# Performance work log

Hardware: AMD Instinct MI355X
Metric: run time of the kernel (lower is better)

## Reference

```python
import jax, jax.numpy as jnp
import numpy as np

EMBED_DIM = 1024
NUM_HEADS = 16
HEAD_DIM = EMBED_DIM // NUM_HEADS


def setup_inputs() -> dict:
    key = jax.random.key(0)
    ks = jax.random.split(key, 5)
    B, T = 2, 2048
    scale = 1.0 / np.sqrt(EMBED_DIM)
    x = jax.random.normal(ks[0], (B, T, EMBED_DIM), dtype=jnp.float32)
    W_qkv = jax.random.normal(ks[1], (EMBED_DIM, 3 * EMBED_DIM), dtype=jnp.float32) * scale
    b_qkv = jnp.zeros((3 * EMBED_DIM,), dtype=jnp.float32)
    W_out = jax.random.normal(ks[2], (EMBED_DIM, EMBED_DIM), dtype=jnp.float32) * scale
    b_out = jnp.zeros((EMBED_DIM,), dtype=jnp.float32)
    return {"x": x, "W_qkv": W_qkv, "b_qkv": b_qkv, "W_out": W_out, "b_out": b_out}


def reference(x, W_qkv, b_qkv, W_out, b_out):
    B, T, E = x.shape
    H, D = NUM_HEADS, HEAD_DIM
    qkv = x @ W_qkv + b_qkv  # [B,T,3E]
    q, k, v = jnp.split(qkv, 3, axis=-1)
    # [B,T,E] -> [B,H,T,D]
    q = q.reshape(B, T, H, D).transpose(0, 2, 1, 3)
    k = k.reshape(B, T, H, D).transpose(0, 2, 1, 3)
    v = v.reshape(B, T, H, D).transpose(0, 2, 1, 3)
    scores = jnp.einsum('bhqd,bhkd->bhqk', q, k) / jnp.sqrt(jnp.float32(D))
    causal = jnp.tril(jnp.ones((T, T), dtype=bool))  # True = keep
    scores = jnp.where(causal[None, None], scores, jnp.float32(-jnp.inf))
    attn = jax.nn.softmax(scores, axis=-1)  # dropout=0.0 (eval mode)
    out = jnp.einsum('bhqk,bhkd->bhqd', attn, v)
    out = out.transpose(0, 2, 1, 3).reshape(B, T, E)
    return out @ W_out + b_out
```

## Files before the change

kernel.cpp:

```cpp
#include <hip/hip_runtime.h>
#include <hip/hip_bf16.h>
#include <stdint.h>

typedef unsigned short u16;
typedef __attribute__((ext_vector_type(8))) short short8;
typedef __attribute__((ext_vector_type(4))) float f32x4;

#define T_SEQ 2048
#define EMB   1024
#define NH    16
#define HD    64

__device__ __forceinline__ u16 f2bf(float f) {
    union { float f; uint32_t u; } x; x.f = f;
    uint32_t u = x.u;
    uint32_t r = u + 0x7fffu + ((u >> 16) & 1u);
    return (u16)(r >> 16);
}

__device__ __forceinline__ uint32_t cvtpk(float a, float b) {
    uint32_t r;
    asm("v_cvt_pk_bf16_f32 %0, %1, %2" : "=v"(r) : "v"(a), "v"(b));
    return r;
}

__device__ __forceinline__ void gld16(const void* g, void* l) {
    __builtin_amdgcn_global_load_lds(
        (const __attribute__((address_space(1))) void*)g,
        (__attribute__((address_space(3))) void*)l, 16, 0, 0);
}

__global__ __launch_bounds__(256) void cast_bf16_kernel(const float* __restrict__ in,
                                                        u16* __restrict__ out, int n4) {
    int i = blockIdx.x * 256 + threadIdx.x;
    if (i < n4) {
        float4 v = ((const float4*)in)[i];
        ((uint2*)out)[i] = make_uint2(cvtpk(v.x, v.y), cvtpk(v.z, v.w));
    }
}

__global__ __launch_bounds__(256) void transpose_cast_kernel(const float* __restrict__ W,
                                                             u16* __restrict__ Wt,
                                                             int K, int N) {
    __shared__ float tile[32][33];
    int n0 = blockIdx.x * 32, k0 = blockIdx.y * 32;
    int tx = threadIdx.x, ty = threadIdx.y;
#pragma unroll
    for (int i = 0; i < 4; i++)
        tile[ty + i * 8][tx] = W[(k0 + ty + i * 8) * N + n0 + tx];
    __syncthreads();
#pragma unroll
    for (int i = 0; i < 4; i++)
        Wt[(size_t)(n0 + ty + i * 8) * K + k0 + tx] = f2bf(tile[tx][ty + i * 8]);
}

__device__ __forceinline__ void gemm_tile(const u16* __restrict__ A, const u16* __restrict__ Bt,
                                          int m0, int n0, f32x4 (&acc)[4][4],
                                          u16* As, u16* Bs, int tid) {
    const int lane = tid & 63;
    const int wid  = tid >> 6;
    const int wr = wid >> 1, wc = wid & 1;
    const int g = lane >> 4, r = lane & 15;
#pragma unroll
    for (int m = 0; m < 4; m++)
#pragma unroll
        for (int n = 0; n < 4; n++) acc[m][n] = (f32x4){0.f, 0.f, 0.f, 0.f};

    const int srow = tid >> 2;
    const int skb  = (tid & 3) * 8;
    const u16* ag = A  + (size_t)(m0 + srow) * 1024 + skb;
    const u16* bg = Bt + (size_t)(n0 + srow) * 1024 + skb;
    char* asl = (char*)As + tid * 16;
    char* bsl = (char*)Bs + tid * 16;

    auto stage = [&](int buf, int kk) {
        gld16(ag + kk,             asl + buf * 8192);
        gld16(ag + kk + 64 * 1024, asl + buf * 8192 + 4096);
        gld16(bg + kk,             bsl + buf * 8192);
        gld16(bg + kk + 64 * 1024, bsl + buf * 8192 + 4096);
    };

    stage(0, 0);
    for (int it = 0; it < 32; ++it) {
        const int cur = it & 1;
        __syncthreads();
        if (it < 31) stage(cur ^ 1, (it + 1) * 32);
        const u16* as = As + cur * 4096;
        const u16* bs = Bs + cur * 4096;
        short8 af[4], bf[4];
#pragma unroll
        for (int m = 0; m < 4; m++) af[m] = *(const short8*)&as[(wr * 64 + m * 16 + r) * 32 + g * 8];
#pragma unroll
        for (int n = 0; n < 4; n++) bf[n] = *(const short8*)&bs[(wc * 64 + n * 16 + r) * 32 + g * 8];
#pragma unroll
        for (int m = 0; m < 4; m++)
#pragma unroll
            for (int n = 0; n < 4; n++)
                acc[m][n] = __builtin_amdgcn_mfma_f32_16x16x32_bf16(af[m], bf[n], acc[m][n], 0, 0, 0);
    }
}

__global__ __launch_bounds__(256) void gemm_qkv_kernel(const u16* __restrict__ A, const u16* __restrict__ Bt,
                                                       const float* __restrict__ bias,
                                                       u16* __restrict__ Qo, u16* __restrict__ Ko,
                                                       u16* __restrict__ VTo) {
    __shared__ __align__(16) u16 As[2][128 * 32];
    __shared__ __align__(16) u16 Bs[2][128 * 32];
    int tid = threadIdx.x;
    int m0 = blockIdx.x * 128, n0 = blockIdx.y * 128;
    f32x4 acc[4][4];
    gemm_tile(A, Bt, m0, n0, acc, &As[0][0], &Bs[0][0], tid);

    int lane = tid & 63, wid = tid >> 6;
    int wr = wid >> 1, wc = wid & 1, g = lane >> 4, r = lane & 15;
#pragma unroll
    for (int m = 0; m < 4; m++) {
#pragma unroll
        for (int n = 0; n < 4; n++) {
            int col = n0 + wc * 64 + n * 16 + r;
            float bv = bias[col];
            int which = col >> 10;
            int e = col & 1023;
            int h = e >> 6, d = e & 63;
            int row0 = m0 + wr * 64 + m * 16 + g * 4;
            int b = row0 >> 11, t0 = row0 & 2047;
            if (which == 2) {
                uint2 pk;
                pk.x = cvtpk(acc[m][n][0] + bv, acc[m][n][1] + bv);
                pk.y = cvtpk(acc[m][n][2] + bv, acc[m][n][3] + bv);
                *(uint2*)&VTo[(((size_t)(b * NH + h)) * HD + d) * T_SEQ + t0] = pk;
            } else {
                u16* dst = which ? Ko : Qo;
                float sc = which ? 1.0f : 0.18033688011112042f;
#pragma unroll
                for (int j = 0; j < 4; j++)
                    dst[(((size_t)(b * NH + h)) * T_SEQ + t0 + j) * HD + d] = f2bf((acc[m][n][j] + bv) * sc);
            }
        }
    }
}

__global__ __launch_bounds__(256) void gemm_out_kernel(const u16* __restrict__ A, const u16* __restrict__ Bt,
                                                       const float* __restrict__ bias,
                                                       float* __restrict__ out) {
    __shared__ __align__(16) u16 As[2][128 * 32];
    __shared__ __align__(16) u16 Bs[2][128 * 32];
    int tid = threadIdx.x;
    int m0 = blockIdx.x * 128, n0 = blockIdx.y * 128;
    f32x4 acc[4][4];
    gemm_tile(A, Bt, m0, n0, acc, &As[0][0], &Bs[0][0], tid);

    int lane = tid & 63, wid = tid >> 6;
    int wr = wid >> 1, wc = wid & 1, g = lane >> 4, r = lane & 15;
#pragma unroll
    for (int m = 0; m < 4; m++) {
#pragma unroll
        for (int n = 0; n < 4; n++) {
            int col = n0 + wc * 64 + n * 16 + r;
            float bv = bias[col];
#pragma unroll
            for (int j = 0; j < 4; j++) {
                int row = m0 + wr * 64 + m * 16 + g * 4 + j;
                out[(size_t)row * 1024 + col] = acc[m][n][j] + bv;
            }
        }
    }
}

__global__ __launch_bounds__(512) void attn_kernel(const u16* __restrict__ Q, const u16* __restrict__ K,
                                                   const u16* __restrict__ VT, u16* __restrict__ O) {
    __shared__ __align__(16) char smem[43008];
    u16* Kl = (u16*)smem;
    u16* Vl = (u16*)(smem + 16384);
    u16 (*Ps)[16][40] = (u16(*)[16][40])(smem + 32768);

    const int tid = threadIdx.x;
    const int lane = tid & 63, wid = tid >> 6;
    const int g = lane >> 4, r = lane & 15;
    const int rg = wid & 3, kh = wid >> 2;
    const int bid = blockIdx.x;
    const int qt = 31 - (bid >> 5);
    const int bh = bid & 31;
    const int b = bh >> 4, h = bh & 15;
    const u16* Qb  = Q  + (size_t)bh * T_SEQ * HD;
    const u16* Kb  = K  + (size_t)bh * T_SEQ * HD;
    const u16* VTb = VT + (size_t)bh * HD * T_SEQ;
    u16 (*myPs)[40] = Ps[wid];
    const float NEGINF = -__builtin_inff();

    int koff[2][2], voff[4];
#pragma unroll
    for (int nt = 0; nt < 2; nt++)
#pragma unroll
        for (int hh = 0; hh < 2; hh++)
            koff[nt][hh] = ((kh * 2 + nt) * 16 + r) * 128 + ((((hh * 4 + g) ^ (r & 7)) << 4));
#pragma unroll
    for (int dt = 0; dt < 4; dt++)
        voff[dt] = (dt * 16 + r) * 128 + ((((kh * 4 + g) ^ (r & 7)) << 4));

    const int srow = tid >> 3;
    const int sm = (tid & 7) ^ (srow & 7);
    const u16* kgp = Kb + srow * HD + sm * 8;
    const u16* vgp = VTb + (size_t)srow * T_SEQ + sm * 8;
    char* kld = (char*)Kl + tid * 16;
    char* vld = (char*)Vl + tid * 16;
    auto stage = [&](int buf, int k0) {
        gld16(kgp + (size_t)k0 * HD, kld + (buf << 13));
        gld16(vgp + k0, vld + (buf << 13));
    };

    short8 onesf;
#pragma unroll
    for (int i = 0; i < 8; i++) onesf[i] = (short)0x3F80;

    const int q0 = qt * 64;
    const int q  = q0 + rg * 16 + r;

    stage(0, 0);

    short8 qf0 = *(const short8*)&Qb[(size_t)q * HD + 8 * g];
    short8 qf1 = *(const short8*)&Qb[(size_t)q * HD + 32 + 8 * g];

    float mrun = -1e30f, srun = 0.f;
    f32x4 o[4];
#pragma unroll
    for (int dt = 0; dt < 4; dt++) o[dt] = (f32x4){0.f, 0.f, 0.f, 0.f};

    for (int kv = 0; kv <= qt; kv++) {
        const int cur = kv & 1;
        const int k0 = kv * 64;
        __syncthreads();
        if (kv < qt) stage(cur ^ 1, k0 + 64);

        const char* kb = (const char*)Kl + (cur << 13);
        const char* vb = (const char*)Vl + (cur << 13);

        f32x4 s[2];
        __builtin_amdgcn_s_setprio(1);
#pragma unroll
        for (int nt = 0; nt < 2; nt++) {
            f32x4 z = (f32x4){0.f, 0.f, 0.f, 0.f};
            z = __builtin_amdgcn_mfma_f32_16x16x32_bf16(*(const short8*)(kb + koff[nt][0]), qf0, z, 0, 0, 0);
            z = __builtin_amdgcn_mfma_f32_16x16x32_bf16(*(const short8*)(kb + koff[nt][1]), qf1, z, 0, 0, 0);
            s[nt] = z;
        }
        __builtin_amdgcn_s_setprio(0);

        if (kv == qt) {
#pragma unroll
            for (int nt = 0; nt < 2; nt++) {
                int kbi = k0 + kh * 32 + nt * 16 + 4 * g;
#pragma unroll
                for (int j = 0; j < 4; j++)
                    if (kbi + j > q) s[nt][j] = NEGINF;
            }
        }

        float t0 = fmaxf(fmaxf(s[0][0], s[0][1]), s[0][2]);
        float t1 = fmaxf(fmaxf(s[0][3], s[1][0]), s[1][1]);
        float t2 = fmaxf(s[1][2], s[1][3]);
        float mt = fmaxf(fmaxf(t0, t1), t2);
        mt = fmaxf(mt, __shfl_xor(mt, 16));
        mt = fmaxf(mt, __shfl_xor(mt, 32));

        if (mt > mrun + 8.f) {
            float corr = __builtin_exp2f(mrun - mt);
            mrun = mt;
            srun *= corr;
#pragma unroll
            for (int dt = 0; dt < 4; dt++)
#pragma unroll
                for (int j = 0; j < 4; j++) o[dt][j] *= corr;
        }

#pragma unroll
        for (int nt = 0; nt < 2; nt++)
#pragma unroll
            for (int j = 0; j < 4; j++)
                s[nt][j] = __builtin_exp2f(s[nt][j] - mrun);

#pragma unroll
        for (int nt = 0; nt < 2; nt++) {
            uint2 pk;
            pk.x = cvtpk(s[nt][0], s[nt][1]);
            pk.y = cvtpk(s[nt][2], s[nt][3]);
            *(uint2*)&myPs[r][nt * 16 + 4 * g] = pk;
        }
        short8 pf = *(short8*)&myPs[r][8 * g];

        __builtin_amdgcn_s_setprio(1);
#pragma unroll
        for (int dt = 0; dt < 4; dt++)
            o[dt] = __builtin_amdgcn_mfma_f32_16x16x32_bf16(*(const short8*)(vb + voff[dt]), pf, o[dt], 0, 0, 0);
        f32x4 zs = (f32x4){0.f, 0.f, 0.f, 0.f};
        zs = __builtin_amdgcn_mfma_f32_16x16x32_bf16(onesf, pf, zs, 0, 0, 0);
        __builtin_amdgcn_s_setprio(0);
        srun += zs[0];
    }

    __syncthreads();
    float* mb = ((float*)smem) + ((rg * 64 + lane) * 18);
    if (kh) {
#pragma unroll
        for (int dt = 0; dt < 4; dt++) *(f32x4*)&mb[dt * 4] = o[dt];
        mb[16] = mrun;
        mb[17] = srun;
    }
    __syncthreads();
    if (!kh) {
        float m1 = mb[16], l1 = mb[17];
        float mm = fmaxf(mrun, m1);
        float c0 = __builtin_exp2f(mrun - mm);
        float c1 = __builtin_exp2f(m1 - mm);
        float inv = 1.f / (srun * c0 + l1 * c1);
        float s0 = c0 * inv, s1 = c1 * inv;
#pragma unroll
        for (int dt = 0; dt < 4; dt++) {
            f32x4 o1 = *(const f32x4*)&mb[dt * 4];
            uint2 pk;
            pk.x = cvtpk(o[dt][0] * s0 + o1[0] * s1, o[dt][1] * s0 + o1[1] * s1);
            pk.y = cvtpk(o[dt][2] * s0 + o1[2] * s1, o[dt][3] * s0 + o1[3] * s1);
            *(uint2*)&O[(((size_t)(b * T_SEQ + q)) * NH + h) * HD + dt * 16 + 4 * g] = pk;
        }
    }
}

extern "C" void kernel_launch(void* const* d_in, const int* in_sizes, int n_in,
                              void* d_out, int out_size, void* d_ws, size_t ws_size,
                              hipStream_t stream) {
    const float* x     = (const float*)d_in[0];
    const float* W_qkv = (const float*)d_in[1];
    const float* b_qkv = (const float*)d_in[2];
    const float* W_out = (const float*)d_in[3];
    const float* b_out = (const float*)d_in[4];
    float* out = (float*)d_out;

    char* ws = (char*)d_ws;
    u16* xb    = (u16*)(ws);
    u16* wqkvt = (u16*)(ws + 8388608);
    u16* woutt = (u16*)(ws + 14680064);
    u16* Qp    = (u16*)(ws + 16777216);
    u16* Kp    = (u16*)(ws + 25165824);
    u16* VTp   = (u16*)(ws + 33554432);
    u16* attnb = (u16*)(ws);

    cast_bf16_kernel<<<4096, 256, 0, stream>>>(x, xb, 1048576);
    transpose_cast_kernel<<<dim3(96, 32), dim3(32, 8), 0, stream>>>(W_qkv, wqkvt, 1024, 3072);
    transpose_cast_kernel<<<dim3(32, 32), dim3(32, 8), 0, stream>>>(W_out, woutt, 1024, 1024);
    gemm_qkv_kernel<<<dim3(32, 24), 256, 0, stream>>>(xb, wqkvt, b_qkv, Qp, Kp, VTp);
    attn_kernel<<<1024, 512, 0, stream>>>(Qp, Kp, VTp, attnb);
    gemm_out_kernel<<<dim3(32, 8), 256, 0, stream>>>(attnb, woutt, b_out, out);
}
```

Before: 126.3 us.

## Fuse prep kernels into one launch and shrink output GEMM tile to 64x128

Merges the x cast and both weight transpose-casts into a single prep kernel, saving two kernel launches. The output projection GEMM moves from 128x128 tiles over 256 blocks to 64x128 tiles over 512 blocks, with its own staging loop, so more CUs are busy on the 4096x1024 output. The attention kernel's shared memory becomes separate typed arrays, and the softmax merge buffer now aliases Kl. The smaller GEMM tile lowers per-block data reuse, and the prep kernel adds branching per block.

```diff
diff --git a/kernel.cpp b/kernel.cpp
--- a/kernel.cpp
+++ b/kernel.cpp
@@ -30,28 +30,31 @@
         (__attribute__((address_space(3))) void*)l, 16, 0, 0);
 }
 
-__global__ __launch_bounds__(256) void cast_bf16_kernel(const float* __restrict__ in,
-                                                        u16* __restrict__ out, int n4) {
-    int i = blockIdx.x * 256 + threadIdx.x;
-    if (i < n4) {
-        float4 v = ((const float4*)in)[i];
-        ((uint2*)out)[i] = make_uint2(cvtpk(v.x, v.y), cvtpk(v.z, v.w));
-    }
-}
-
-__global__ __launch_bounds__(256) void transpose_cast_kernel(const float* __restrict__ W,
-                                                             u16* __restrict__ Wt,
-                                                             int K, int N) {
+__global__ __launch_bounds__(256) void prep_kernel(const float* __restrict__ x, u16* __restrict__ xb,
+                                                   const float* __restrict__ Wq, u16* __restrict__ Wqt,
+                                                   const float* __restrict__ Wo, u16* __restrict__ Wot) {
     __shared__ float tile[32][33];
-    int n0 = blockIdx.x * 32, k0 = blockIdx.y * 32;
-    int tx = threadIdx.x, ty = threadIdx.y;
+    const int bid = blockIdx.x;
+    if (bid < 4096) {
+        int i = bid * 256 + threadIdx.x;
+        float4 v = ((const float4*)x)[i];
+        ((uint2*)xb)[i] = make_uint2(cvtpk(v.x, v.y), cvtpk(v.z, v.w));
+        return;
+    }
+    int t = bid - 4096;
+    const float* W; u16* Wt; int N;
+    if (t < 3072) { W = Wq; Wt = Wqt; N = 3072; }
+    else          { W = Wo; Wt = Wot; N = 1024; t -= 3072; }
+    const int ntiles = N >> 5;
+    const int n0 = (t % ntiles) * 32, k0 = (t / ntiles) * 32;
+    const int tx = threadIdx.x & 31, ty = threadIdx.x >> 5;
 #pragma unroll
     for (int i = 0; i < 4; i++)
-        tile[ty + i * 8][tx] = W[(k0 + ty + i * 8) * N + n0 + tx];
+        tile[ty + i * 8][tx] = W[(size_t)(k0 + ty + i * 8) * N + n0 + tx];
     __syncthreads();
 #pragma unroll
     for (int i = 0; i < 4; i++)
-        Wt[(size_t)(n0 + ty + i * 8) * K + k0 + tx] = f2bf(tile[tx][ty + i * 8]);
+        Wt[(size_t)(n0 + ty + i * 8) * 1024 + k0 + tx] = f2bf(tile[tx][ty + i * 8]);
 }
 
 __device__ __forceinline__ void gemm_tile(const u16* __restrict__ A, const u16* __restrict__ Bt,
@@ -143,24 +146,60 @@
 __global__ __launch_bounds__(256) void gemm_out_kernel(const u16* __restrict__ A, const u16* __restrict__ Bt,
                                                        const float* __restrict__ bias,
                                                        float* __restrict__ out) {
-    __shared__ __align__(16) u16 As[2][128 * 32];
+    __shared__ __align__(16) u16 As[2][64 * 32];
     __shared__ __align__(16) u16 Bs[2][128 * 32];
-    int tid = threadIdx.x;
-    int m0 = blockIdx.x * 128, n0 = blockIdx.y * 128;
-    f32x4 acc[4][4];
-    gemm_tile(A, Bt, m0, n0, acc, &As[0][0], &Bs[0][0], tid);
-
-    int lane = tid & 63, wid = tid >> 6;
-    int wr = wid >> 1, wc = wid & 1, g = lane >> 4, r = lane & 15;
+    const int tid = threadIdx.x;
+    const int m0 = blockIdx.x * 64, n0 = blockIdx.y * 128;
+    const int lane = tid & 63, wid = tid >> 6;
+    const int g = lane >> 4, r = lane & 15;
+
+    f32x4 acc[4][2];
+#pragma unroll
+    for (int m = 0; m < 4; m++)
+#pragma unroll
+        for (int n = 0; n < 2; n++) acc[m][n] = (f32x4){0.f, 0.f, 0.f, 0.f};
+
+    const int srow = tid >> 2;
+    const int skb  = (tid & 3) * 8;
+    const u16* ag = A  + (size_t)(m0 + srow) * 1024 + skb;
+    const u16* bg = Bt + (size_t)(n0 + srow) * 1024 + skb;
+    char* asl = (char*)As + tid * 16;
+    char* bsl = (char*)Bs + tid * 16;
+
+    auto stage = [&](int buf, int kk) {
+        gld16(ag + kk,             asl + buf * 4096);
+        gld16(bg + kk,             bsl + buf * 8192);
+        gld16(bg + kk + 64 * 1024, bsl + buf * 8192 + 4096);
+    };
+
+    stage(0, 0);
+    for (int it = 0; it < 32; ++it) {
+        const int cur = it & 1;
+        __syncthreads();
+        if (it < 31) stage(cur ^ 1, (it + 1) * 32);
+        const u16* as = &As[cur][0];
+        const u16* bs = &Bs[cur][0];
+        short8 af[4], bf[2];
+#pragma unroll
+        for (int m = 0; m < 4; m++) af[m] = *(const short8*)&as[(m * 16 + r) * 32 + g * 8];
+#pragma unroll
+        for (int n = 0; n < 2; n++) bf[n] = *(const short8*)&bs[(wid * 32 + n * 16 + r) * 32 + g * 8];
+#pragma unroll
+        for (int m = 0; m < 4; m++)
+#pragma unroll
+            for (int n = 0; n < 2; n++)
+                acc[m][n] = __builtin_amdgcn_mfma_f32_16x16x32_bf16(af[m], bf[n], acc[m][n], 0, 0, 0);
+    }
+
 #pragma unroll
     for (int m = 0; m < 4; m++) {
 #pragma unroll
-        for (int n = 0; n < 4; n++) {
-            int col = n0 + wc * 64 + n * 16 + r;
+        for (int n = 0; n < 2; n++) {
+            int col = n0 + wid * 32 + n * 16 + r;
             float bv = bias[col];
 #pragma unroll
             for (int j = 0; j < 4; j++) {
-                int row = m0 + wr * 64 + m * 16 + g * 4 + j;
+                int row = m0 + m * 16 + g * 4 + j;
                 out[(size_t)row * 1024 + col] = acc[m][n][j] + bv;
             }
         }
@@ -169,10 +208,9 @@
 
 __global__ __launch_bounds__(512) void attn_kernel(const u16* __restrict__ Q, const u16* __restrict__ K,
                                                    const u16* __restrict__ VT, u16* __restrict__ O) {
-    __shared__ __align__(16) char smem[43008];
-    u16* Kl = (u16*)smem;
-    u16* Vl = (u16*)(smem + 16384);
-    u16 (*Ps)[16][40] = (u16(*)[16][40])(smem + 32768);
+    __shared__ __align__(16) u16 Kl[2][64 * 64];
+    __shared__ __align__(16) u16 Vl[2][64 * 64];
+    __shared__ __align__(16) u16 Ps[8][16][40];
 
     const int tid = threadIdx.x;
     const int lane = tid & 63, wid = tid >> 6;
@@ -299,7 +337,7 @@
     }
 
     __syncthreads();
-    float* mb = ((float*)smem) + ((rg * 64 + lane) * 18);
+    float* mb = ((float*)&Kl[0][0]) + ((rg * 64 + lane) * 18);
     if (kh) {
 #pragma unroll
         for (int dt = 0; dt < 4; dt++) *(f32x4*)&mb[dt * 4] = o[dt];
@@ -344,10 +382,8 @@
     u16* VTp   = (u16*)(ws + 33554432);
     u16* attnb = (u16*)(ws);
 
-    cast_bf16_kernel<<<4096, 256, 0, stream>>>(x, xb, 1048576);
-    transpose_cast_kernel<<<dim3(96, 32), dim3(32, 8), 0, stream>>>(W_qkv, wqkvt, 1024, 3072);
-    transpose_cast_kernel<<<dim3(32, 32), dim3(32, 8), 0, stream>>>(W_out, woutt, 1024, 1024);
+    prep_kernel<<<8192, 256, 0, stream>>>(x, xb, W_qkv, wqkvt, W_out, woutt);
     gemm_qkv_kernel<<<dim3(32, 24), 256, 0, stream>>>(xb, wqkvt, b_qkv, Qp, Kp, VTp);
     attn_kernel<<<1024, 512, 0, stream>>>(Qp, Kp, VTp, attnb);
-    gemm_out_kernel<<<dim3(32, 8), 256, 0, stream>>>(attnb, woutt, b_out, out);
-}
+    gemm_out_kernel<<<dim3(64, 8), 256, 0, stream>>>(attnb, woutt, b_out, out);
+}
```

After: 118.7 us. -6.0%, faster.
